# Kernel optimization log

Hardware: AMD Instinct MI355X
Metric: run time of the kernel (lower is better)

## Reference

```python
import jax, jax.numpy as jnp
import numpy as np

B, T, S, E, H = 2, 2048, 2048, 1024, 16
HD = E // H  # 64


def setup_inputs() -> dict:
    key = jax.random.key(0)
    ks = jax.random.split(key, 13)
    sc = 1.0 / np.sqrt(E)
    inp = {
        "q": jax.random.normal(ks[0], (B, T, E), jnp.float32),
        "k": jax.random.normal(ks[1], (B, S, E), jnp.float32),
        "v": jax.random.normal(ks[2], (B, S, E), jnp.float32),
        "attn_mask": jax.random.randint(ks[3], (T, S), 0, 2, jnp.int32),
        "Wq": jax.random.normal(ks[4], (E, E), jnp.float32) * sc,
        "bq": jax.random.normal(ks[5], (E,), jnp.float32) * 0.01,
        "Wk": jax.random.normal(ks[6], (E, E), jnp.float32) * sc,
        "bk": jax.random.normal(ks[7], (E,), jnp.float32) * 0.01,
        "Wv": jax.random.normal(ks[8], (E, E), jnp.float32) * sc,
        "bv": jax.random.normal(ks[9], (E,), jnp.float32) * 0.01,
        "Wo": jax.random.normal(ks[10], (E, E), jnp.float32) * sc,
        "bo": jax.random.normal(ks[11], (E,), jnp.float32) * 0.01,
    }
    return inp


def reference(q, k, v, attn_mask, Wq, bq, Wk, bk, Wv, bv, Wo, bo):
    bsz, tgt_len, embed_dim = q.shape
    src_len = k.shape[1]
    # torch Linear: x @ W.T + b
    qh = (q @ Wq.T + bq).reshape(bsz, tgt_len, H, HD).transpose(0, 2, 1, 3)  # [B,H,T,HD]
    kh = (k @ Wk.T + bk).reshape(bsz, src_len, H, HD).transpose(0, 2, 1, 3)  # [B,H,S,HD]
    vh = (v @ Wv.T + bv).reshape(bsz, src_len, H, HD).transpose(0, 2, 1, 3)  # [B,H,S,HD]
    scale = 1.0 / jnp.sqrt(jnp.asarray(HD, qh.dtype))
    attn = jnp.einsum('bhtd,bhsd->bhts', qh, kh) * scale  # [B,H,T,S]
    attn = jnp.where(attn_mask != 0, jnp.asarray(-10000.0, attn.dtype), attn)
    attn = jax.nn.softmax(attn, axis=-1)
    out = jnp.einsum('bhts,bhsd->bhtd', attn, vh)  # [B,H,T,HD]
    out = out.transpose(0, 2, 1, 3).reshape(bsz, tgt_len, embed_dim)
    return out @ Wo.T + bo
```

## Files before the change

kernel.cpp:

```cpp
#include <hip/hip_runtime.h>
#include <hip/hip_bf16.h>
#include <math.h>

#define QSCALE 0.18033688011112042f

typedef __attribute__((ext_vector_type(4))) float f32x4;
typedef __attribute__((ext_vector_type(8))) short bf16x8;
typedef __attribute__((ext_vector_type(4))) short bf16x4;
typedef __attribute__((ext_vector_type(4))) float float4_t;
typedef __attribute__((ext_vector_type(4))) int int4_t;
typedef __attribute__((ext_vector_type(2))) unsigned int uint2_t;
typedef __attribute__((ext_vector_type(2))) unsigned long long u64x2;

typedef const __attribute__((address_space(1))) void gbl_cvoid;
typedef __attribute__((address_space(3))) void lds_void;

static __device__ __forceinline__ void gload16(const void* g, void* l){
  __builtin_amdgcn_global_load_lds((gbl_cvoid*)g, (lds_void*)l, 16, 0, 0);
}

static __device__ __forceinline__ unsigned short f2b(float f){
  unsigned int u = __builtin_bit_cast(unsigned int, f);
  u = (u + 0x7FFFu + ((u >> 16) & 1u)) >> 16;
  return (unsigned short)u;
}

static __device__ __forceinline__ unsigned int cvtpk_bf16(float a, float b){
  unsigned int r;
  asm("v_cvt_pk_bf16_f32 %0, %1, %2" : "=v"(r) : "v"(a), "v"(b));
  return r;
}

#if defined(__has_builtin)
#if __has_builtin(__builtin_amdgcn_exp2f)
#define EXP2R __builtin_amdgcn_exp2f
#endif
#endif
#ifndef EXP2R
#define EXP2R exp2f
#endif

struct CvtArgs { const float* src[7]; unsigned short* dst[7]; };

__global__ __launch_bounds__(256) void cvt_kernel(CvtArgs a, const int* __restrict__ mask,
                                                  unsigned long long* __restrict__ mout){
  int y = blockIdx.y;
  if (y == 7){
    if (blockIdx.x >= 256) return;
    int w = blockIdx.x * 256 + threadIdx.x;
    const int* p = mask + (size_t)w * 64;
    unsigned long long bits = 0ull;
    #pragma unroll
    for (int j = 0; j < 64; j += 4){
      int4_t v4 = *(const int4_t*)(p + j);
      if (v4[0]) bits |= (1ull << (j + 0));
      if (v4[1]) bits |= (1ull << (j + 1));
      if (v4[2]) bits |= (1ull << (j + 2));
      if (v4[3]) bits |= (1ull << (j + 3));
    }
    mout[w] = bits;
    return;
  }
  int n4 = (y < 3) ? (4194304/4) : (1048576/4);
  int idx = blockIdx.x * 256 + threadIdx.x;
  if (idx >= n4) return;
  float4_t v = *(const float4_t*)(a.src[y] + (size_t)idx * 4);
  bf16x4 b; b[0]=(short)f2b(v[0]); b[1]=(short)f2b(v[1]); b[2]=(short)f2b(v[2]); b[3]=(short)f2b(v[3]);
  *(bf16x4*)(a.dst[y] + (size_t)idx * 4) = b;
}

struct GemmArgs { const unsigned short* A[3]; const unsigned short* W[3];
                  const float* bias[3]; void* C[3]; };

__global__ __launch_bounds__(256) void gemm_qkv_kernel(GemmArgs ga)
{
  __shared__ unsigned short As[2*128*32];
  __shared__ unsigned short Ws[2*128*32];
  const int tid = threadIdx.x, lane = tid & 63, wid = tid >> 6;
  const int bid = blockIdx.x;
  const int nid = (bid & 7) * 96 + (bid >> 3);
  const int m0  = (nid / 24) * 128;
  const int rest = nid % 24;
  const int sel = rest >> 3;
  const int n0  = (rest & 7) * 128;
  const unsigned short* A = ga.A[sel];
  const unsigned short* W = ga.W[sel];
  const float* bias = ga.bias[sel];
  const int wm = wid >> 1, wn = wid & 1;
  const int r16 = lane & 15, kg = lane >> 4;
  const int phA = (kg ^ ((r16 >> 1) & 3)) * 8;
  const int sRow = tid >> 2;
  const int sL   = (tid & 3) ^ ((tid >> 3) & 3);

  f32x4 acc[4][4];
  const f32x4 z4 = {0.f, 0.f, 0.f, 0.f};
  #pragma unroll
  for (int i = 0; i < 4; ++i)
    #pragma unroll
    for (int j = 0; j < 4; ++j) acc[i][j] = z4;

  #pragma unroll
  for (int i = 0; i < 2; ++i){
    gload16(A + (size_t)(m0 + i*64 + sRow) * 1024 + sL * 8, (char*)As + i*4096 + wid*1024);
    gload16(W + (size_t)(n0 + i*64 + sRow) * 1024 + sL * 8, (char*)Ws + i*4096 + wid*1024);
  }

#define GSTEP(CUR, IT)                                                                \
  {                                                                                   \
    if ((IT) < 31) {                                                                  \
      const int k1 = ((IT) + 1) * 32;                                                 \
      _Pragma("unroll")                                                               \
      for (int i = 0; i < 2; ++i){                                                    \
        gload16(A + (size_t)(m0 + i*64 + sRow) * 1024 + k1 + sL * 8,                  \
                (char*)As + ((CUR) ^ 1) * 8192 + i*4096 + wid*1024);                  \
        gload16(W + (size_t)(n0 + i*64 + sRow) * 1024 + k1 + sL * 8,                  \
                (char*)Ws + ((CUR) ^ 1) * 8192 + i*4096 + wid*1024);                  \
      }                                                                               \
      asm volatile("s_waitcnt vmcnt(4)" ::: "memory");                                \
    } else {                                                                          \
      asm volatile("s_waitcnt vmcnt(0)" ::: "memory");                                \
    }                                                                                 \
    __builtin_amdgcn_sched_barrier(0);                                                \
    __builtin_amdgcn_s_barrier();            \
    bf16x8 af[4], wf[4];                                                              \
    _Pragma("unroll")                                                                 \
    for (int mi = 0; mi < 4; ++mi)                                                    \
      af[mi] = *(const bf16x8*)(As + (CUR)*4096 + (wm*64 + mi*16 + r16)*32 + phA);    \
    _Pragma("unroll")                                                                 \
    for (int ni = 0; ni < 4; ++ni)                                                    \
      wf[ni] = *(const bf16x8*)(Ws + (CUR)*4096 + (wn*64 + ni*16 + r16)*32 + phA);    \
    __builtin_amdgcn_s_setprio(1);                                                    \
    _Pragma("unroll")                                                                 \
    for (int mi = 0; mi < 4; ++mi)                                                    \
      _Pragma("unroll")                                                               \
      for (int ni = 0; ni < 4; ++ni)                                                  \
        acc[mi][ni] = __builtin_amdgcn_mfma_f32_16x16x32_bf16(af[mi], wf[ni],         \
                                                              acc[mi][ni], 0, 0, 0); \
    __builtin_amdgcn_s_setprio(0);                                                    \
    __builtin_amdgcn_s_barrier();            \
  }

  for (int ii = 0; ii < 16; ++ii) {
    GSTEP(0, 2 * ii)
    GSTEP(1, 2 * ii + 1)
  }
#undef GSTEP

  #pragma unroll
  for (int mi = 0; mi < 4; ++mi){
    #pragma unroll
    for (int ni = 0; ni < 4; ++ni){
      int m = m0 + wm*64 + mi*16 + kg*4;
      int n = n0 + wn*64 + ni*16 + r16;
      float bv = bias[n];
      if (sel == 2){
        int bb = m >> 11, t = m & 2047, hh = n >> 6, d = n & 63;
        bf16x4 pk;
        #pragma unroll
        for (int r = 0; r < 4; ++r) pk[r] = (short)f2b(acc[mi][ni][r] + bv);
        *(bf16x4*)&((unsigned short*)ga.C[2])[((size_t)(bb*16 + hh) * 64 + d) * 2048 + t] = pk;
      } else {
        #pragma unroll
        for (int r = 0; r < 4; ++r){
          float v = acc[mi][ni][r] + bv;
          if (sel == 0) v *= QSCALE;
          int mm = m + r;
          int bb = mm >> 11, t = mm & 2047, hh = n >> 6, d = n & 63;
          ((unsigned short*)ga.C[sel])[(((size_t)(bb*16 + hh) * 2048 + t) << 6) + d] = f2b(v);
        }
      }
    }
  }
}

__global__ __launch_bounds__(256) void gemm_o_kernel(const unsigned short* __restrict__ A,
    const unsigned short* __restrict__ W, const float* __restrict__ bias,
    float* __restrict__ C)
{
  __shared__ unsigned short As[2*64*32];
  __shared__ unsigned short Ws[2*128*32];
  const int tid = threadIdx.x, lane = tid & 63, wid = tid >> 6;
  const int bid = blockIdx.x;
  const int nid = (bid & 7) * 64 + (bid >> 3);
  const int m0 = (nid >> 3) * 64;
  const int n0 = (nid & 7) * 128;
  const int wm = wid >> 1, wn = wid & 1;
  const int r16 = lane & 15, kg = lane >> 4;
  const int phA = (kg ^ ((r16 >> 1) & 3)) * 8;
  const int sRow = tid >> 2;
  const int sL   = (tid & 3) ^ ((tid >> 3) & 3);

  f32x4 acc[2][4];
  const f32x4 z4 = {0.f, 0.f, 0.f, 0.f};
  #pragma unroll
  for (int i = 0; i < 2; ++i)
    #pragma unroll
    for (int j = 0; j < 4; ++j) acc[i][j] = z4;

  gload16(A + (size_t)(m0 + sRow) * 1024 + sL * 8, (char*)As + wid*1024);
  #pragma unroll
  for (int i = 0; i < 2; ++i)
    gload16(W + (size_t)(n0 + i*64 + sRow) * 1024 + sL * 8, (char*)Ws + i*4096 + wid*1024);

#define OSTEP(CUR, IT)                                                                \
  {                                                                                   \
    if ((IT) < 31) {                                                                  \
      const int k1 = ((IT) + 1) * 32;                                                 \
      gload16(A + (size_t)(m0 + sRow) * 1024 + k1 + sL * 8,                           \
              (char*)As + ((CUR) ^ 1) * 4096 + wid*1024);                             \
      _Pragma("unroll")                                                               \
      for (int i = 0; i < 2; ++i)                                                     \
        gload16(W + (size_t)(n0 + i*64 + sRow) * 1024 + k1 + sL * 8,                  \
                (char*)Ws + ((CUR) ^ 1) * 8192 + i*4096 + wid*1024);                  \
      asm volatile("s_waitcnt vmcnt(3)" ::: "memory");                                \
    } else {                                                                          \
      asm volatile("s_waitcnt vmcnt(0)" ::: "memory");                                \
    }                                                                                 \
    __builtin_amdgcn_sched_barrier(0);                                                \
    __builtin_amdgcn_s_barrier();                                                     \
    bf16x8 af[2], wf[4];                                                              \
    _Pragma("unroll")                                                                 \
    for (int mi = 0; mi < 2; ++mi)                                                    \
      af[mi] = *(const bf16x8*)(As + (CUR)*2048 + (wm*32 + mi*16 + r16)*32 + phA);    \
    _Pragma("unroll")                                                                 \
    for (int ni = 0; ni < 4; ++ni)                                                    \
      wf[ni] = *(const bf16x8*)(Ws + (CUR)*4096 + (wn*64 + ni*16 + r16)*32 + phA);    \
    __builtin_amdgcn_s_setprio(1);                                                    \
    _Pragma("unroll")                                                                 \
    for (int mi = 0; mi < 2; ++mi)                                                    \
      _Pragma("unroll")                                                               \
      for (int ni = 0; ni < 4; ++ni)                                                  \
        acc[mi][ni] = __builtin_amdgcn_mfma_f32_16x16x32_bf16(af[mi], wf[ni],         \
                                                              acc[mi][ni], 0, 0, 0); \
    __builtin_amdgcn_s_setprio(0);                                                    \
    __builtin_amdgcn_s_barrier();                                                     \
  }

  for (int ii = 0; ii < 16; ++ii) {
    OSTEP(0, 2 * ii)
    OSTEP(1, 2 * ii + 1)
  }
#undef OSTEP

  #pragma unroll
  for (int mi = 0; mi < 2; ++mi){
    #pragma unroll
    for (int ni = 0; ni < 4; ++ni){
      int m = m0 + wm*32 + mi*16 + kg*4;
      int n = n0 + wn*64 + ni*16 + r16;
      float bv = bias[n];
      #pragma unroll
      for (int r = 0; r < 4; ++r)
        C[(size_t)(m + r) * 1024 + n] = acc[mi][ni][r] + bv;
    }
  }
}

__global__ __launch_bounds__(512) void attn_kernel(const unsigned short* __restrict__ qh,
    const unsigned short* __restrict__ kh, const unsigned short* __restrict__ vhT,
    const unsigned long long* __restrict__ mbits, unsigned short* __restrict__ attnout)
{
  __shared__ short Ks[2][2][64][64];
  __shared__ short Vs[2][2][64][64];
  __shared__ short Ps[128][64];
  const int tid = threadIdx.x, lane = tid & 63, wid = tid >> 6;
  const int bid = blockIdx.x;
  const int nid = (bid & 7) * 64 + (bid >> 3);
  const int bh = nid >> 4;
  const int b = bh >> 4, h = bh & 15;
  const int t0 = (nid & 15) * 128;
  const int tw = t0 + wid * 16;
  const int r16 = lane & 15, kg = lane >> 4;
  const int x7 = r16 & 7;
  const int ph0 = (kg ^ x7) * 8;
  const int ph1 = ((kg + 4) ^ x7) * 8;
  const int sR = tid >> 3;
  const int sL = (tid & 7) ^ (sR & 7);

  const unsigned short* kbase = kh + (size_t)bh * 2048 * 64;
  const unsigned short* vtb   = vhT + (size_t)bh * 64 * 2048;
  const unsigned short* qbase = qh + ((size_t)bh * 2048 + tw) * 64;

  bf16x8 aq[2];
  aq[0] = *(const bf16x8*)(qbase + (size_t)r16 * 64 + kg * 8);
  aq[1] = *(const bf16x8*)(qbase + (size_t)r16 * 64 + 32 + kg * 8);

  const short ob = (short)0x3F80;
  const bf16x8 ones8 = {ob, ob, ob, ob, ob, ob, ob, ob};

  f32x4 o[4], o5;
  const f32x4 z4 = {0.f, 0.f, 0.f, 0.f};
  #pragma unroll
  for (int df = 0; df < 4; ++df) o[df] = z4;
  o5 = z4;

  const unsigned long long* mrow = mbits + (size_t)(tw + r16) * 32;
  const size_t koff = (size_t)sR * 64 + sL * 8;
  const size_t voff = (size_t)sR * 2048 + sL * 8;

  #pragma unroll
  for (int i = 0; i < 2; ++i){
    gload16(kbase + (size_t)i * 4096 + koff, (char*)Ks + i * 8192 + wid * 1024);
    gload16(vtb + voff + i * 64,            (char*)Vs + i * 8192 + wid * 1024);
  }
  u64x2 mw = *(const u64x2*)(mrow);
  __syncthreads();

#define ATTN_STEP(CUR, IT)                                                            \
  {                                                                                   \
    u64x2 mwn = mw;                                                                   \
    if ((IT) < 15) {                                                                  \
      const unsigned short* kc = kbase + (size_t)((IT) + 1) * 8192;                   \
      const unsigned short* vc = vtb + (size_t)((IT) + 1) * 128;                      \
      _Pragma("unroll")                                                               \
      for (int i = 0; i < 2; ++i){                                                    \
        gload16(kc + (size_t)i * 4096 + koff,                                         \
                (char*)Ks + ((CUR) ^ 1) * 16384 + i * 8192 + wid * 1024);             \
        gload16(vc + voff + i * 64,                                                   \
                (char*)Vs + ((CUR) ^ 1) * 16384 + i * 8192 + wid * 1024);             \
      }                                                                               \
      mwn = *(const u64x2*)(mrow + 2 * ((IT) + 1));                                   \
    }                                                                                 \
    _Pragma("unroll")                                                                 \
    for (int sub = 0; sub < 2; ++sub){                                                \
      f32x4 sfr[4];                                                                   \
      __builtin_amdgcn_s_setprio(1);                                                  \
      _Pragma("unroll")                                                               \
      for (int sb = 0; sb < 4; ++sb){                                                 \
        bf16x8 bk0 = *(const bf16x8*)&Ks[CUR][sub][sb*16 + r16][ph0];                 \
        bf16x8 bk1 = *(const bf16x8*)&Ks[CUR][sub][sb*16 + r16][ph1];                 \
        f32x4 z = z4;                                                                 \
        z = __builtin_amdgcn_mfma_f32_16x16x32_bf16(bk0, aq[0], z, 0, 0, 0);          \
        z = __builtin_amdgcn_mfma_f32_16x16x32_bf16(bk1, aq[1], z, 0, 0, 0);          \
        sfr[sb] = z;                                                                  \
      }                                                                               \
      __builtin_amdgcn_s_setprio(0);                                                  \
      {                                                                               \
        unsigned long long mk = (~mw[sub]) >> (kg * 4);                 \
        unsigned int wlo = (unsigned int)mk;                                          \
        unsigned int whi = (unsigned int)(mk >> 32);                                  \
        _Pragma("unroll")                                                             \
        for (int sb = 0; sb < 4; ++sb){                                               \
          unsigned int wd = (sb < 2) ? wlo : whi;                                     \
          float pf[4];                                                                \
          _Pragma("unroll")                                                           \
          for (int r = 0; r < 4; ++r){                                                \
            const int pos = (sb & 1) * 16 + r;                                        \
            unsigned int msk = (unsigned int)((int)(wd << (31 - pos)) >> 31);         \
            float e = EXP2R(sfr[sb][r]);                                              \
            pf[r] = __builtin_bit_cast(float,                                         \
                      __builtin_bit_cast(unsigned int, e) & msk);                     \
          }                                                                           \
          unsigned int lo = cvtpk_bf16(pf[0], pf[1]);                                 \
          unsigned int hi = cvtpk_bf16(pf[2], pf[3]);                                 \
          int phys = (sb * 2 + (kg >> 1)) ^ x7;                                       \
          uint2_t pk; pk[0] = lo; pk[1] = hi;                                         \
          *(uint2_t*)&Ps[wid*16 + r16][phys * 8 + (kg & 1) * 4] = pk;                 \
        }                                                                             \
      }                                                                               \
      bf16x8 pa0 = *(const bf16x8*)&Ps[wid*16 + r16][ph0];                            \
      bf16x8 pa1 = *(const bf16x8*)&Ps[wid*16 + r16][ph1];                            \
      __builtin_amdgcn_s_setprio(1);                                                  \
      _Pragma("unroll")                                                               \
      for (int df = 0; df < 4; ++df){                                                 \
        bf16x8 bv0 = *(const bf16x8*)&Vs[CUR][sub][df*16 + r16][ph0];                 \
        bf16x8 bv1 = *(const bf16x8*)&Vs[CUR][sub][df*16 + r16][ph1];                 \
        o[df] = __builtin_amdgcn_mfma_f32_16x16x32_bf16(pa0, bv0, o[df], 0, 0, 0);    \
        o[df] = __builtin_amdgcn_mfma_f32_16x16x32_bf16(pa1, bv1, o[df], 0, 0, 0);    \
      }                                                                               \
      o5 = __builtin_amdgcn_mfma_f32_16x16x32_bf16(pa0, ones8, o5, 0, 0, 0);          \
      o5 = __builtin_amdgcn_mfma_f32_16x16x32_bf16(pa1, ones8, o5, 0, 0, 0);          \
      __builtin_amdgcn_s_setprio(0);                                                  \
    }                                                                                 \
    __syncthreads();                                                                  \
    mw = mwn;                                                                         \
  }

  for (int ii = 0; ii < 8; ++ii) {
    ATTN_STEP(0, 2 * ii)
    ATTN_STEP(1, 2 * ii + 1)
  }
#undef ATTN_STEP

  float lv0 = 1.0f / o5[0];
  float lv1 = 1.0f / o5[1];
  float lv2 = 1.0f / o5[2];
  float lv3 = 1.0f / o5[3];
  #pragma unroll
  for (int df = 0; df < 4; ++df){
    int col = h*64 + df*16 + r16;
    int t = tw + kg*4;
    attnout[(size_t)(b * 2048 + t + 0) * 1024 + col] = (short)f2b(o[df][0] * lv0);
    attnout[(size_t)(b * 2048 + t + 1) * 1024 + col] = (short)f2b(o[df][1] * lv1);
    attnout[(size_t)(b * 2048 + t + 2) * 1024 + col] = (short)f2b(o[df][2] * lv2);
    attnout[(size_t)(b * 2048 + t + 3) * 1024 + col] = (short)f2b(o[df][3] * lv3);
  }
}

extern "C" void kernel_launch(void* const* d_in, const int* in_sizes, int n_in,
                              void* d_out, int out_size, void* d_ws, size_t ws_size,
                              hipStream_t stream) {
  const float* q    = (const float*)d_in[0];
  const float* k    = (const float*)d_in[1];
  const float* v    = (const float*)d_in[2];
  const int*   mask = (const int*)d_in[3];
  const float* Wq = (const float*)d_in[4];  const float* bq = (const float*)d_in[5];
  const float* Wk = (const float*)d_in[6];  const float* bk = (const float*)d_in[7];
  const float* Wv = (const float*)d_in[8];  const float* bv = (const float*)d_in[9];
  const float* Wo = (const float*)d_in[10]; const float* bo = (const float*)d_in[11];

  char* ws = (char*)d_ws;
  unsigned short* qb   = (unsigned short*)(ws);
  unsigned short* kb   = (unsigned short*)(ws + 8388608);
  unsigned short* vb   = (unsigned short*)(ws + 16777216);
  unsigned short* Wqb  = (unsigned short*)(ws + 25165824);
  unsigned short* Wkb  = (unsigned short*)(ws + 27262976);
  unsigned short* Wvb  = (unsigned short*)(ws + 29360128);
  unsigned short* Wob  = (unsigned short*)(ws + 31457280);
  unsigned short* qhd  = (unsigned short*)(ws + 33554432);
  unsigned short* khd  = (unsigned short*)(ws + 41943040);
  unsigned short* vhT  = (unsigned short*)(ws + 50331648);
  unsigned long long* mbits = (unsigned long long*)(ws + 58720256);
  unsigned short* attno = qb;

  CvtArgs ca;
  ca.src[0]=q;  ca.dst[0]=qb;  ca.src[1]=k;  ca.dst[1]=kb;  ca.src[2]=v;  ca.dst[2]=vb;
  ca.src[3]=Wq; ca.dst[3]=Wqb; ca.src[4]=Wk; ca.dst[4]=Wkb;
  ca.src[5]=Wv; ca.dst[5]=Wvb; ca.src[6]=Wo; ca.dst[6]=Wob;
  cvt_kernel<<<dim3(4096, 8), 256, 0, stream>>>(ca, mask, mbits);

  GemmArgs g0;
  g0.A[0]=qb; g0.A[1]=kb; g0.A[2]=vb;
  g0.W[0]=Wqb; g0.W[1]=Wkb; g0.W[2]=Wvb;
  g0.bias[0]=bq; g0.bias[1]=bk; g0.bias[2]=bv;
  g0.C[0]=qhd; g0.C[1]=khd; g0.C[2]=vhT;
  gemm_qkv_kernel<<<768, 256, 0, stream>>>(g0);

  attn_kernel<<<512, 512, 0, stream>>>(qhd, khd, vhT, mbits, attno);

  gemm_o_kernel<<<512, 256, 0, stream>>>(attno, Wob, bo, (float*)d_out);
}
```

Before: 127.4 us.

## Fuse fp32-to-bf16 activation conversion into QKV GEMM A-tile loads

The separate conversion pass over q, k and v to bf16 is removed. The QKV GEMM now streams fp32 activations straight into LDS with a swizzled layout and converts them to bf16 fragments in registers before the MFMA. This drops a full write-then-read round trip of the activations through global memory and shrinks the conversion kernel to the weights and mask only. In exchange the A tiles double in LDS size and global traffic inside the GEMM, and each K-step does extra VALU conversion work.

New measurement: 153.6 us. 20.6% more time.

```diff
diff --git a/kernel.cpp b/kernel.cpp
--- a/kernel.cpp
+++ b/kernel.cpp
@@ -10,6 +10,7 @@
 typedef __attribute__((ext_vector_type(4))) float float4_t;
 typedef __attribute__((ext_vector_type(4))) int int4_t;
 typedef __attribute__((ext_vector_type(2))) unsigned int uint2_t;
+typedef __attribute__((ext_vector_type(4))) unsigned int uint4_t;
 typedef __attribute__((ext_vector_type(2))) unsigned long long u64x2;
 
 typedef const __attribute__((address_space(1))) void gbl_cvoid;
@@ -29,6 +30,23 @@
   unsigned int r;
   asm("v_cvt_pk_bf16_f32 %0, %1, %2" : "=v"(r) : "v"(a), "v"(b));
   return r;
+}
+
+static __device__ __forceinline__ unsigned int packbf(float fa, float fb){
+  unsigned int ua = __builtin_bit_cast(unsigned int, fa);
+  unsigned int ub = __builtin_bit_cast(unsigned int, fb);
+  ua += 0x7FFFu + ((ua >> 16) & 1u);
+  ub += 0x7FFFu + ((ub >> 16) & 1u);
+  return __builtin_amdgcn_perm(ub, ua, 0x07060302u);
+}
+
+static __device__ __forceinline__ bf16x8 cvt_frag(f32x4 a0, f32x4 a1){
+  uint4_t u;
+  u[0] = packbf(a0[0], a0[1]);
+  u[1] = packbf(a0[2], a0[3]);
+  u[2] = packbf(a1[0], a1[1]);
+  u[3] = packbf(a1[2], a1[3]);
+  return __builtin_bit_cast(bf16x8, u);
 }
 
 #if defined(__has_builtin)
@@ -40,12 +58,12 @@
 #define EXP2R exp2f
 #endif
 
-struct CvtArgs { const float* src[7]; unsigned short* dst[7]; };
+struct CvtArgs { const float* src[4]; unsigned short* dst[4]; };
 
 __global__ __launch_bounds__(256) void cvt_kernel(CvtArgs a, const int* __restrict__ mask,
                                                   unsigned long long* __restrict__ mout){
   int y = blockIdx.y;
-  if (y == 7){
+  if (y == 4){
     if (blockIdx.x >= 256) return;
     int w = blockIdx.x * 256 + threadIdx.x;
     const int* p = mask + (size_t)w * 64;
@@ -61,20 +79,18 @@
     mout[w] = bits;
     return;
   }
-  int n4 = (y < 3) ? (4194304/4) : (1048576/4);
   int idx = blockIdx.x * 256 + threadIdx.x;
-  if (idx >= n4) return;
   float4_t v = *(const float4_t*)(a.src[y] + (size_t)idx * 4);
   bf16x4 b; b[0]=(short)f2b(v[0]); b[1]=(short)f2b(v[1]); b[2]=(short)f2b(v[2]); b[3]=(short)f2b(v[3]);
   *(bf16x4*)(a.dst[y] + (size_t)idx * 4) = b;
 }
 
-struct GemmArgs { const unsigned short* A[3]; const unsigned short* W[3];
+struct GemmArgs { const float* A[3]; const unsigned short* W[3];
                   const float* bias[3]; void* C[3]; };
 
 __global__ __launch_bounds__(256) void gemm_qkv_kernel(GemmArgs ga)
 {
-  __shared__ unsigned short As[2*128*32];
+  __shared__ float As[2*128*32];
   __shared__ unsigned short Ws[2*128*32];
   const int tid = threadIdx.x, lane = tid & 63, wid = tid >> 6;
   const int bid = blockIdx.x;
@@ -83,14 +99,17 @@
   const int rest = nid % 24;
   const int sel = rest >> 3;
   const int n0  = (rest & 7) * 128;
-  const unsigned short* A = ga.A[sel];
+  const float* A = ga.A[sel];
   const unsigned short* W = ga.W[sel];
   const float* bias = ga.bias[sel];
   const int wm = wid >> 1, wn = wid & 1;
   const int r16 = lane & 15, kg = lane >> 4;
-  const int phA = (kg ^ ((r16 >> 1) & 3)) * 8;
+  const int x7f = r16 & 7;
+  const int phW = (kg ^ ((r16 >> 1) & 3)) * 8;
+  const int aRow = tid >> 3;
+  const int aLc  = (tid & 7) ^ (aRow & 7);
   const int sRow = tid >> 2;
-  const int sL   = (tid & 3) ^ ((tid >> 3) & 3);
+  const int sLw  = (tid & 3) ^ ((tid >> 3) & 3);
 
   f32x4 acc[4][4];
   const f32x4 z4 = {0.f, 0.f, 0.f, 0.f};
@@ -100,35 +119,43 @@
     for (int j = 0; j < 4; ++j) acc[i][j] = z4;
 
   #pragma unroll
-  for (int i = 0; i < 2; ++i){
-    gload16(A + (size_t)(m0 + i*64 + sRow) * 1024 + sL * 8, (char*)As + i*4096 + wid*1024);
-    gload16(W + (size_t)(n0 + i*64 + sRow) * 1024 + sL * 8, (char*)Ws + i*4096 + wid*1024);
-  }
+  for (int i = 0; i < 4; ++i)
+    gload16(A + (size_t)(m0 + i*32 + aRow) * 1024 + aLc * 4,
+            (char*)As + i*4096 + tid*16);
+  #pragma unroll
+  for (int i = 0; i < 2; ++i)
+    gload16(W + (size_t)(n0 + i*64 + sRow) * 1024 + sLw * 8,
+            (char*)Ws + i*4096 + wid*1024);
 
 #define GSTEP(CUR, IT)                                                                \
   {                                                                                   \
     if ((IT) < 31) {                                                                  \
       const int k1 = ((IT) + 1) * 32;                                                 \
       _Pragma("unroll")                                                               \
-      for (int i = 0; i < 2; ++i){                                                    \
-        gload16(A + (size_t)(m0 + i*64 + sRow) * 1024 + k1 + sL * 8,                  \
-                (char*)As + ((CUR) ^ 1) * 8192 + i*4096 + wid*1024);                  \
-        gload16(W + (size_t)(n0 + i*64 + sRow) * 1024 + k1 + sL * 8,                  \
+      for (int i = 0; i < 4; ++i)                                                     \
+        gload16(A + (size_t)(m0 + i*32 + aRow) * 1024 + k1 + aLc * 4,                 \
+                (char*)As + ((CUR) ^ 1) * 16384 + i*4096 + tid*16);                   \
+      _Pragma("unroll")                                                               \
+      for (int i = 0; i < 2; ++i)                                                     \
+        gload16(W + (size_t)(n0 + i*64 + sRow) * 1024 + k1 + sLw * 8,                 \
                 (char*)Ws + ((CUR) ^ 1) * 8192 + i*4096 + wid*1024);                  \
-      }                                                                               \
-      asm volatile("s_waitcnt vmcnt(4)" ::: "memory");                                \
+      asm volatile("s_waitcnt vmcnt(6)" ::: "memory");                                \
     } else {                                                                          \
       asm volatile("s_waitcnt vmcnt(0)" ::: "memory");                                \
     }                                                                                 \
     __builtin_amdgcn_sched_barrier(0);                                                \
-    __builtin_amdgcn_s_barrier();            \
+    __builtin_amdgcn_s_barrier();             \
     bf16x8 af[4], wf[4];                                                              \
     _Pragma("unroll")                                                                 \
-    for (int mi = 0; mi < 4; ++mi)                                                    \
-      af[mi] = *(const bf16x8*)(As + (CUR)*4096 + (wm*64 + mi*16 + r16)*32 + phA);    \
+    for (int mi = 0; mi < 4; ++mi){                                                   \
+      const int row = wm*64 + mi*16 + r16;                                            \
+      f32x4 a0 = *(const f32x4*)(As + (CUR)*4096 + row*32 + ((2*kg    ) ^ x7f)*4);    \
+      f32x4 a1 = *(const f32x4*)(As + (CUR)*4096 + row*32 + ((2*kg + 1) ^ x7f)*4);    \
+      af[mi] = cvt_frag(a0, a1);                                                      \
+    }                                                                                 \
     _Pragma("unroll")                                                                 \
     for (int ni = 0; ni < 4; ++ni)                                                    \
-      wf[ni] = *(const bf16x8*)(Ws + (CUR)*4096 + (wn*64 + ni*16 + r16)*32 + phA);    \
+      wf[ni] = *(const bf16x8*)(Ws + (CUR)*4096 + (wn*64 + ni*16 + r16)*32 + phW);    \
     __builtin_amdgcn_s_setprio(1);                                                    \
     _Pragma("unroll")                                                                 \
     for (int mi = 0; mi < 4; ++mi)                                                    \
@@ -410,9 +437,7 @@
   const float* Wo = (const float*)d_in[10]; const float* bo = (const float*)d_in[11];
 
   char* ws = (char*)d_ws;
-  unsigned short* qb   = (unsigned short*)(ws);
-  unsigned short* kb   = (unsigned short*)(ws + 8388608);
-  unsigned short* vb   = (unsigned short*)(ws + 16777216);
+  unsigned short* attno = (unsigned short*)(ws);
   unsigned short* Wqb  = (unsigned short*)(ws + 25165824);
   unsigned short* Wkb  = (unsigned short*)(ws + 27262976);
   unsigned short* Wvb  = (unsigned short*)(ws + 29360128);
@@ -421,16 +446,14 @@
   unsigned short* khd  = (unsigned short*)(ws + 41943040);
   unsigned short* vhT  = (unsigned short*)(ws + 50331648);
   unsigned long long* mbits = (unsigned long long*)(ws + 58720256);
-  unsigned short* attno = qb;
 
   CvtArgs ca;
-  ca.src[0]=q;  ca.dst[0]=qb;  ca.src[1]=k;  ca.dst[1]=kb;  ca.src[2]=v;  ca.dst[2]=vb;
-  ca.src[3]=Wq; ca.dst[3]=Wqb; ca.src[4]=Wk; ca.dst[4]=Wkb;
-  ca.src[5]=Wv; ca.dst[5]=Wvb; ca.src[6]=Wo; ca.dst[6]=Wob;
-  cvt_kernel<<<dim3(4096, 8), 256, 0, stream>>>(ca, mask, mbits);
+  ca.src[0]=Wq; ca.dst[0]=Wqb; ca.src[1]=Wk; ca.dst[1]=Wkb;
+  ca.src[2]=Wv; ca.dst[2]=Wvb; ca.src[3]=Wo; ca.dst[3]=Wob;
+  cvt_kernel<<<dim3(1024, 5), 256, 0, stream>>>(ca, mask, mbits);
 
   GemmArgs g0;
-  g0.A[0]=qb; g0.A[1]=kb; g0.A[2]=vb;
+  g0.A[0]=q; g0.A[1]=k; g0.A[2]=v;
   g0.W[0]=Wqb; g0.W[1]=Wkb; g0.W[2]=Wvb;
   g0.bias[0]=bq; g0.bias[1]=bk; g0.bias[2]=bv;
   g0.C[0]=qhd; g0.C[1]=khd; g0.C[2]=vhT;
```
